# Performance work log

Hardware: AMD Instinct MI355X
Metric: run time of the kernel (lower is better)

## Reference

```python
import jax, jax.numpy as jnp
import numpy as np
from jax import lax

B = 16           # graphs per batch
N_PER = 4096     # points per graph (equal-sized graphs)
C_IN = 32        # in_channels
RATIO = 0.25
MAX_NBR = 32     # max_num_neighbors in radius()


def _xavier(key, fan_in, fan_out):
    lim = np.sqrt(6.0 / (fan_in + fan_out)).astype(np.float32)
    return jax.random.uniform(key, (fan_in, fan_out), jnp.float32, -lim, lim)


def setup_inputs() -> dict:
    key = jax.random.key(0)
    ks = jax.random.split(key, 16)
    x = jax.random.normal(ks[0], (B * N_PER, C_IN), jnp.float32)
    pos = jax.random.uniform(ks[1], (B * N_PER, 3), jnp.float32) * 20.0
    batch = jnp.repeat(jnp.arange(B, dtype=jnp.int64), N_PER)
    p = {
        'x': x, 'pos': pos, 'batch': batch,
        'scaler_mean': jnp.zeros((1, C_IN), jnp.float32),
        'scaler_std': jnp.ones((1, C_IN), jnp.float32),
        # SA1: Linear(32+3,64) -> Sigmoid -> Linear(64,128)
        'sa1_w1': _xavier(ks[2], C_IN + 3, 64), 'sa1_b1': jnp.zeros((64,), jnp.float32),
        'sa1_w2': _xavier(ks[3], 64, 128),      'sa1_b2': jnp.zeros((128,), jnp.float32),
        # SA2: Linear(128+3,128) -> Sigmoid -> Linear(128,256)
        'sa2_w1': _xavier(ks[4], 128 + 3, 128), 'sa2_b1': jnp.zeros((128,), jnp.float32),
        'sa2_w2': _xavier(ks[5], 128, 256),     'sa2_b2': jnp.zeros((256,), jnp.float32),
        # Global SA: Linear(256+3,256) -> Sigmoid -> Linear(256,512)
        'g_w1': _xavier(ks[6], 256 + 3, 256),   'g_b1': jnp.zeros((256,), jnp.float32),
        'g_w2': _xavier(ks[7], 256, 512),       'g_b2': jnp.zeros((512,), jnp.float32),
        # fc: Linear(512,256) -> Sigmoid -> Linear(256,128)
        'fc_w1': _xavier(ks[8], 512, 256),      'fc_b1': jnp.zeros((256,), jnp.float32),
        'fc_w2': _xavier(ks[9], 256, 128),      'fc_b2': jnp.zeros((128,), jnp.float32),
    }
    return p


def _fps(pos, k):
    # Farthest point sampling, deterministic start at index 0. pos: [B, n, 3] -> idx [B, k]
    pos = lax.stop_gradient(pos)
    d0 = jnp.sum((pos - pos[:, :1, :]) ** 2, -1)  # [B, n] dist^2 to start point

    def step(mind, _):
        nxt = jnp.argmax(mind, axis=1)                                  # [B]
        p = jnp.take_along_axis(pos, nxt[:, None, None], axis=1)        # [B,1,3]
        mind = jnp.minimum(mind, jnp.sum((pos - p) ** 2, -1))
        return mind, nxt

    _, rest = lax.scan(step, d0, None, length=k - 1)                    # [k-1, B]
    start = jnp.zeros((1, pos.shape[0]), rest.dtype)
    return jnp.concatenate([start, rest], 0).T                          # [B, k]


def _gather_nbr(v, nbr):
    # v: [B, n, C], nbr: [B, k, MAX_NBR] -> [B, k, MAX_NBR, C]
    return jax.vmap(lambda vb, nb: vb[nb])(v, nbr)


def _sa_module(x, pos, w1, b1, w2, b2, ratio, r):
    # PointNetConv (max aggregation) over a radius graph from FPS centers.
    Bb, n, _ = x.shape
    k = int(n * ratio)
    idx = _fps(pos, k)                                                  # [B, k]
    pos_dst = jnp.take_along_axis(pos, idx[:, :, None], axis=1)         # [B, k, 3]
    d2 = jnp.sum((pos_dst[:, :, None, :] - pos[:, None, :, :]) ** 2, -1)  # [B,k,n]
    masked = jnp.where(d2 <= r * r, d2, jnp.inf)
    negv, nbr = lax.top_k(-masked, MAX_NBR)                             # nearest <=32 within radius
    valid = jnp.isfinite(negv)                                          # [B,k,32]
    x_j = _gather_nbr(x, nbr)                                           # [B,k,32,C]
    rel = _gather_nbr(pos, nbr) - pos_dst[:, :, None, :]                # pos_j - pos_i
    feat = jnp.concatenate([x_j, rel], axis=-1)
    msg = jax.nn.sigmoid(feat @ w1 + b1) @ w2 + b2                      # [B,k,32,2h]
    msg = jnp.where(valid[..., None], msg, -jnp.inf)
    agg = jnp.max(msg, axis=2)                                          # max aggregation
    agg = jnp.where(jnp.isfinite(agg), agg, 0.0)  # (self is always a neighbor, defensive)
    return jax.nn.relu(agg), pos_dst


def reference(x, pos, batch, scaler_mean, scaler_std,
              sa1_w1, sa1_b1, sa1_w2, sa1_b2,
              sa2_w1, sa2_b1, sa2_w2, sa2_b2,
              g_w1, g_b1, g_w2, g_b2,
              fc_w1, fc_b1, fc_w2, fc_b2):
    x = (x - scaler_mean) / scaler_std
    xb = x.reshape(B, N_PER, -1)      # batch is sorted with N_PER points per graph
    pb = pos.reshape(B, N_PER, 3)
    xb, pb = _sa_module(xb, pb, sa1_w1, sa1_b1, sa1_w2, sa1_b2, RATIO, 2.0)
    xb, pb = _sa_module(xb, pb, sa2_w1, sa2_b1, sa2_w2, sa2_b2, RATIO, 4.0)
    # GlobalSAModule: relu(nn(cat[x, pos])) then global max pool
    h = jnp.concatenate([xb, pb], axis=-1)
    h = jax.nn.relu(jax.nn.sigmoid(h @ g_w1 + g_b1) @ g_w2 + g_b2)      # [B, 256, 512]
    g = jnp.max(h, axis=1)                                              # [B, 512]
    out = jax.nn.sigmoid(g @ fc_w1 + fc_b1) @ fc_w2 + fc_b2
    return jax.nn.relu(out)                                             # last_act='relu'
```

## Files before the change

kernel.cpp:

```cpp
#include <hip/hip_runtime.h>
#include <hip/hip_bf16.h>
#include <math.h>

namespace {

constexpr int NB   = 16;
constexpr int N1   = 4096;
constexpr int K1   = 1024;
constexpr int K2   = 256;
constexpr int MAXN = 32;
constexpr int RCAP = 448;

__device__ __forceinline__ float sigmoidf_(float x) {
  return 1.0f / (1.0f + __expf(-x));
}

__device__ __forceinline__ float readlane_f(float v, int l) {
  return __int_as_float(__builtin_amdgcn_readlane(__float_as_int(v), l));
}


#define FPS_DPP_STEP(CTRL)                                                     \
  {                                                                            \
    const unsigned olo =                                                       \
        (unsigned)__builtin_amdgcn_update_dpp(0, (int)lo, (CTRL), 0xF, 0xF, true); \
    const unsigned ohi =                                                       \
        (unsigned)__builtin_amdgcn_update_dpp(0, (int)hi, (CTRL), 0xF, 0xF, true); \
    const unsigned long long o = ((unsigned long long)ohi << 32) | olo;        \
    const unsigned long long cur = ((unsigned long long)hi << 32) | lo;        \
    if (o > cur) { lo = olo; hi = ohi; }                                       \
  }

template<int NPT>
__device__ __forceinline__ void fps_level(
    const float* __restrict__ sx, const float* __restrict__ sy,
    const float* __restrict__ sz, int k,
    float* __restrict__ selx, float* __restrict__ sely,
    float* __restrict__ selz,
    unsigned long long (*red)[4]) {
  const int t = threadIdx.x;
  const int lane = t & 63, wave = t >> 6;
  float px[NPT], py[NPT], pz[NPT], mind[NPT];
  unsigned niv[NPT];
  const float c0x = sx[0], c0y = sy[0], c0z = sz[0];
  unsigned long long best = 0;
#pragma unroll
  for (int i = 0; i < NPT; i++) {
    const int p = i * 256 + t;
    niv[i] = ~(unsigned)p;
    px[i] = sx[p]; py[i] = sy[p]; pz[i] = sz[p];
    const float dx = px[i] - c0x, dy = py[i] - c0y, dz = pz[i] - c0z;
    const float d2 = dx * dx + dy * dy + dz * dz;
    mind[i] = d2;
    const unsigned long long cand =
        ((unsigned long long)__float_as_uint(d2) << 32) | niv[i];
    if (cand > best) best = cand;
  }
  if (t == 0) { selx[0] = c0x; sely[0] = c0y; selz[0] = c0z; }
  for (int it = 1; it < k; it++) {
    unsigned lo = (unsigned)best, hi = (unsigned)(best >> 32);
    FPS_DPP_STEP(0x111)
    FPS_DPP_STEP(0x112)
    FPS_DPP_STEP(0x114)
    FPS_DPP_STEP(0x118)
    FPS_DPP_STEP(0x142)
    FPS_DPP_STEP(0x143)
    const int par = it & 1;
    if (lane == 63) red[par][wave] = ((unsigned long long)hi << 32) | lo;
    __syncthreads();
    const unsigned long long w0 = red[par][0], w1 = red[par][1];
    const unsigned long long w2 = red[par][2], w3 = red[par][3];
    const unsigned long long m01 = w0 > w1 ? w0 : w1;
    const unsigned long long m23 = w2 > w3 ? w2 : w3;
    const unsigned long long win = m01 > m23 ? m01 : m23;
    const int p = (int)(~(unsigned)win);
    const float nx = sx[p], ny = sy[p], nz = sz[p];
    if (t == 0) { selx[it] = nx; sely[it] = ny; selz[it] = nz; }
    best = 0;
#pragma unroll
    for (int i = 0; i < NPT; i++) {
      const float dx = px[i] - nx, dy = py[i] - ny, dz = pz[i] - nz;
      const float d2 = dx * dx + dy * dy + dz * dz;
      const float m = fminf(mind[i], d2);
      mind[i] = m;
      const unsigned long long cand =
          ((unsigned long long)__float_as_uint(m) << 32) | niv[i];
      if (cand > best) best = cand;
    }
  }
}

#undef FPS_DPP_STEP

__global__ __launch_bounds__(256) void fps_l1_kernel(
    const float* __restrict__ pos, float* __restrict__ posd1,
    unsigned int* __restrict__ gout) {
  __shared__ float sx[N1], sy[N1], sz[N1];
  __shared__ float s2x[K1], s2y[K1], s2z[K1];
  __shared__ __align__(16) unsigned long long red[2][4];
  const int b = blockIdx.x;
  const int t = threadIdx.x;
  gout[b * 512 + t] = 0u;
  gout[b * 512 + t + 256] = 0u;
  const float* pb = pos + (size_t)b * N1 * 3;
  for (int p = t; p < N1; p += 256) {
    sx[p] = pb[p * 3 + 0]; sy[p] = pb[p * 3 + 1]; sz[p] = pb[p * 3 + 2];
  }
  __syncthreads();
  fps_level<N1 / 256>(sx, sy, sz, K1, s2x, s2y, s2z, red);
  __syncthreads();
  float* o1 = posd1 + (size_t)b * K1 * 3;
  for (int i = t; i < K1; i += 256) {
    o1[i * 3 + 0] = s2x[i]; o1[i * 3 + 1] = s2y[i]; o1[i * 3 + 2] = s2z[i];
  }
}

struct RadSmem {
  float candd[4][RCAP];
  int   candi[4][RCAP];
};

template<int N>
__device__ __forceinline__ void radius_body(
    const float* __restrict__ pts, const float* __restrict__ ctr,
    int K, int CSTR, float r2, int* __restrict__ nbr,
    int* __restrict__ cnt_out, RadSmem& sm, int rb) {
  const int t = threadIdx.x;
  const int lane = t & 63, wave = t >> 6;
  const int bpg = K / 4;
  const int b = rb / bpg;
  const int ci = (rb % bpg) * 4 + wave;
  const float* pb = pts + (size_t)b * N * 3;
  const size_t cbase = ((size_t)b * CSTR + ci) * 3;
  const float cx = ctr[cbase + 0], cy = ctr[cbase + 1], cz = ctr[cbase + 2];
  int total = 0;
  for (int base = 0; base < N; base += 64) {
    const int p = base + lane;
    const float dx = pb[p * 3 + 0] - cx;
    const float dy = pb[p * 3 + 1] - cy;
    const float dz = pb[p * 3 + 2] - cz;
    const float d2 = dx * dx + dy * dy + dz * dz;
    const bool pred = d2 <= r2;
    const unsigned long long m = __ballot(pred);
    if (pred) {
      const int slot = total + __popcll(m & ((1ull << lane) - 1ull));
      if (slot < RCAP) { sm.candd[wave][slot] = d2; sm.candi[wave][slot] = p; }
    }
    total += __popcll(m);
  }
  if (total > RCAP) total = RCAP;
  int* nbp = nbr + ((size_t)b * K + ci) * MAXN;
  if (total <= MAXN) {
    if (lane < total) nbp[lane] = sm.candi[wave][lane];
  } else {
    for (int jj = 0; jj < MAXN; jj++) {
      float bvd = INFINITY; int bvi = 0x7fffffff; int bslot = 0;
      for (int s = lane; s < total; s += 64) {
        const float d = sm.candd[wave][s];
        const int i = sm.candi[wave][s];
        if (d < bvd || (d == bvd && i < bvi)) { bvd = d; bvi = i; bslot = s; }
      }
#pragma unroll
      for (int off = 32; off; off >>= 1) {
        const float od = __shfl_xor(bvd, off);
        const int   oi = __shfl_xor(bvi, off);
        const int   os = __shfl_xor(bslot, off);
        if (od < bvd || (od == bvd && oi < bvi)) { bvd = od; bvi = oi; bslot = os; }
      }
      if (lane == 0) { nbp[jj] = bvi; sm.candd[wave][bslot] = INFINITY; }
    }
  }
  if (lane == 0) cnt_out[(size_t)b * K + ci] = (total < MAXN) ? total : MAXN;
}

__global__ __launch_bounds__(256) void rad12_kernel(
    const float* __restrict__ pos, const float* __restrict__ posd1,
    int* __restrict__ nbr1, int* __restrict__ cnt1,
    int* __restrict__ nbr2, int* __restrict__ cnt2) {
  constexpr int NR1 = NB * K1 / 4;
  __shared__ __align__(16) RadSmem r;
  if (blockIdx.x < (unsigned)NR1) {
    radius_body<N1>(pos, posd1, K1, K1, 4.0f, nbr1, cnt1, r, blockIdx.x);
  } else {
    radius_body<K1>(posd1, posd1, K2, K1, 16.0f, nbr2, cnt2, r,
                    blockIdx.x - NR1);
  }
}

template<int CIN_T, int H, int COUT, bool SCALE>
__device__ __forceinline__ void sa_conv_body(
    const float* __restrict__ xin, const float* __restrict__ pts,
    const float* __restrict__ ctr, const int* __restrict__ nbr,
    const int* __restrict__ cnt,
    const float* __restrict__ w1, const float* __restrict__ b1,
    const float* __restrict__ w2, const float* __restrict__ b2,
    const float* __restrict__ smean, const float* __restrict__ sstd,
    int N, int K, int CSTR, float* __restrict__ xout,
    float* part , int bk) {
  constexpr int FIN  = CIN_T + 3;
  constexpr int KREG = (FIN + 63) / 64;
  constexpr int HREG = H / 64;
  constexpr int CREG = COUT / 64;
  constexpr int RPW  = MAXN / 4;
  const int t = threadIdx.x, lane = t & 63, wave = t >> 6;
  const int b = bk / K;
  const int V = cnt[bk];
  float m[CREG];
#pragma unroll
  for (int ck = 0; ck < CREG; ck++) m[ck] = -INFINITY;
  if (V > wave * RPW) {
    const int* nb = nbr + (size_t)bk * MAXN;
    const size_t crow = (size_t)b * CSTR + (bk - b * K);
    const float ctrx = ctr[crow * 3 + 0];
    const float ctry = ctr[crow * 3 + 1];
    const float ctrz = ctr[crow * 3 + 2];
    float sm = 0.0f, sd = 1.0f;
    if (SCALE && lane < CIN_T) { sm = smean[lane]; sd = sstd[lane]; }
    float fr[RPW][KREG];
#pragma unroll
    for (int r = 0; r < RPW; r++) {
      const int j = wave * RPW + r;
      const int p = (j < V) ? nb[j] : nb[0];
#pragma unroll
      for (int k2 = 0; k2 < KREG; k2++) {
        const int f = k2 * 64 + lane;
        float v = 0.0f;
        if (f < CIN_T) {
          v = xin[((size_t)b * N + p) * CIN_T + f];
          if constexpr (SCALE) v = (v - sm) / sd;
        } else if (f < FIN) {
          const int d = f - CIN_T;
          const float pv = pts[((size_t)b * N + p) * 3 + d];
          v = pv - (d == 0 ? ctrx : (d == 1 ? ctry : ctrz));
        }
        fr[r][k2] = v;
      }
    }
    float hh[RPW][HREG];
    {
      float acc[RPW][HREG];
#pragma unroll
      for (int r = 0; r < RPW; r++)
#pragma unroll
        for (int q = 0; q < HREG; q++) acc[r][q] = 0.0f;
#pragma unroll
      for (int k2 = 0; k2 < KREG; k2++) {
        const int lim = (FIN - k2 * 64) < 64 ? (FIN - k2 * 64) : 64;
        for (int fl = 0; fl < lim; fl++) {
          const int f = k2 * 64 + fl;
          float wv[HREG];
          if constexpr (HREG == 1) {
            wv[0] = w1[(size_t)f * H + lane];
          } else {
            const float2 w = *reinterpret_cast<const float2*>(
                &w1[(size_t)f * H + lane * 2]);
            wv[0] = w.x; wv[1] = w.y;
          }
#pragma unroll
          for (int r = 0; r < RPW; r++) {
            const float s = readlane_f(fr[r][k2], fl);
#pragma unroll
            for (int q = 0; q < HREG; q++) acc[r][q] = fmaf(s, wv[q], acc[r][q]);
          }
        }
      }
#pragma unroll
      for (int q = 0; q < HREG; q++) {
        const float bb = b1[lane * HREG + q];
#pragma unroll
        for (int r = 0; r < RPW; r++) hh[r][q] = sigmoidf_(acc[r][q] + bb);
      }
    }
    float acc2[RPW][CREG];
#pragma unroll
    for (int r = 0; r < RPW; r++)
#pragma unroll
      for (int q = 0; q < CREG; q++) acc2[r][q] = 0.0f;
    for (int hl = 0; hl < 64; hl++) {
#pragma unroll
      for (int q1 = 0; q1 < HREG; q1++) {
        const int h = hl * HREG + q1;
        float wv[CREG];
        if constexpr (CREG == 2) {
          const float2 w = *reinterpret_cast<const float2*>(
              &w2[(size_t)h * COUT + lane * 2]);
          wv[0] = w.x; wv[1] = w.y;
        } else {
          const float4 w = *reinterpret_cast<const float4*>(
              &w2[(size_t)h * COUT + lane * 4]);
          wv[0] = w.x; wv[1] = w.y; wv[2] = w.z; wv[3] = w.w;
        }
#pragma unroll
        for (int r = 0; r < RPW; r++) {
          const float s = readlane_f(hh[r][q1], hl);
#pragma unroll
          for (int q = 0; q < CREG; q++) acc2[r][q] = fmaf(s, wv[q], acc2[r][q]);
        }
      }
    }
#pragma unroll
    for (int r = 0; r < RPW; r++) {
      if (wave * RPW + r < V) {
#pragma unroll
        for (int q = 0; q < CREG; q++) m[q] = fmaxf(m[q], acc2[r][q]);
      }
    }
  }
#pragma unroll
  for (int q = 0; q < CREG; q++) part[wave * COUT + lane * CREG + q] = m[q];
  __syncthreads();
  if (t < COUT) {
    const float mm = fmaxf(fmaxf(part[0 * COUT + t], part[1 * COUT + t]),
                           fmaxf(part[2 * COUT + t], part[3 * COUT + t]));
    const float o = mm + b2[t];
    xout[(size_t)bk * COUT + t] = o > 0.0f ? o : 0.0f;
  }
}

__global__ __launch_bounds__(256) void conv1_kernel(
    const float* __restrict__ x, const float* __restrict__ pos,
    const float* __restrict__ posd1, const int* __restrict__ nbr1,
    const int* __restrict__ cnt1,
    const float* __restrict__ s1w1, const float* __restrict__ s1b1,
    const float* __restrict__ s1w2, const float* __restrict__ s1b2,
    const float* __restrict__ smean, const float* __restrict__ sstd,
    float* __restrict__ x1) {
  __shared__ __align__(16) float part[4 * 128];
  sa_conv_body<32, 64, 128, true>(x, pos, posd1, nbr1, cnt1,
                                  s1w1, s1b1, s1w2, s1b2, smean, sstd,
                                  N1, K1, K1, x1, part, blockIdx.x);
}

__global__ __launch_bounds__(256) void conv2_kernel(
    const float* __restrict__ x1, const float* __restrict__ posd1,
    const int* __restrict__ nbr2, const int* __restrict__ cnt2,
    const float* __restrict__ s2w1, const float* __restrict__ s2b1,
    const float* __restrict__ s2w2, const float* __restrict__ s2b2,
    float* __restrict__ x2) {
  __shared__ __align__(16) float part[4 * 256];
  sa_conv_body<128, 128, 256, false>(x1, posd1, posd1, nbr2, cnt2,
                                     s2w1, s2b1, s2w2, s2b2, nullptr, nullptr,
                                     K1, K2, K1, x2, part, blockIdx.x);
}

__global__ __launch_bounds__(256) void global_sa_kernel(
    const float* __restrict__ x2, const float* __restrict__ posd1,
    const float* __restrict__ gw1, const float* __restrict__ gb1,
    const float* __restrict__ gw2, const float* __restrict__ gb2,
    unsigned int* __restrict__ gout) {
  __shared__ float fin[4][259];
  __shared__ float s[4][256];
  const int t = threadIdx.x;
  const int blk = blockIdx.x;
  const int b = blk / 64;
  const int p0 = (blk % 64) * 4;
  for (int item = t; item < 4 * 259; item += 256) {
    const int p = item / 259, f = item - p * 259;
    const float v = (f < 256)
        ? x2[((size_t)b * 256 + p0 + p) * 256 + f]
        : posd1[((size_t)b * K1 + p0 + p) * 3 + (f - 256)];
    fin[p][f] = v;
  }
  __syncthreads();
  float acc[4] = {0.f, 0.f, 0.f, 0.f};
  for (int f = 0; f < 259; f++) {
    const float w = gw1[f * 256 + t];
#pragma unroll
    for (int p = 0; p < 4; p++) acc[p] = fmaf(fin[p][f], w, acc[p]);
  }
  const float bb = gb1[t];
#pragma unroll
  for (int p = 0; p < 4; p++) s[p][t] = sigmoidf_(acc[p] + bb);
  __syncthreads();
  float a0[4] = {0.f, 0.f, 0.f, 0.f}, a1[4] = {0.f, 0.f, 0.f, 0.f};
  for (int h = 0; h < 256; h++) {
    const float w0 = gw2[h * 512 + t];
    const float w1v = gw2[h * 512 + t + 256];
#pragma unroll
    for (int p = 0; p < 4; p++) {
      a0[p] = fmaf(s[p][h], w0, a0[p]);
      a1[p] = fmaf(s[p][h], w1v, a1[p]);
    }
  }
  const float b0 = gb2[t], b1v = gb2[t + 256];
  float m0 = 0.0f, m1 = 0.0f;
#pragma unroll
  for (int p = 0; p < 4; p++) {
    m0 = fmaxf(m0, fmaxf(a0[p] + b0, 0.0f));
    m1 = fmaxf(m1, fmaxf(a1[p] + b1v, 0.0f));
  }
  atomicMax(&gout[b * 512 + t], __float_as_uint(m0));
  atomicMax(&gout[b * 512 + t + 256], __float_as_uint(m1));
}

__global__ __launch_bounds__(256) void fc_kernel(
    const unsigned int* __restrict__ g,
    const float* __restrict__ fw1, const float* __restrict__ fb1,
    const float* __restrict__ fw2, const float* __restrict__ fb2,
    float* __restrict__ out) {
  __shared__ float gv[512];
  __shared__ float s[256];
  const int b = blockIdx.x, t = threadIdx.x;
  gv[t] = __uint_as_float(g[b * 512 + t]);
  gv[t + 256] = __uint_as_float(g[b * 512 + t + 256]);
  __syncthreads();
  float acc = 0.0f;
  for (int h = 0; h < 512; h++) acc = fmaf(gv[h], fw1[h * 256 + t], acc);
  s[t] = sigmoidf_(acc + fb1[t]);
  __syncthreads();
  if (t < 128) {
    float a2 = 0.0f;
    for (int h = 0; h < 256; h++) a2 = fmaf(s[h], fw2[h * 128 + t], a2);
    const float o = a2 + fb2[t];
    out[b * 128 + t] = o > 0.0f ? o : 0.0f;
  }
}

}

extern "C" void kernel_launch(void* const* d_in, const int* in_sizes, int n_in,
                              void* d_out, int out_size, void* d_ws, size_t ws_size,
                              hipStream_t stream) {
  (void)in_sizes; (void)n_in; (void)out_size; (void)ws_size;
  const float* x     = (const float*)d_in[0];
  const float* pos   = (const float*)d_in[1];
  const float* smean = (const float*)d_in[3];
  const float* sstd  = (const float*)d_in[4];
  const float* s1w1  = (const float*)d_in[5];
  const float* s1b1  = (const float*)d_in[6];
  const float* s1w2  = (const float*)d_in[7];
  const float* s1b2  = (const float*)d_in[8];
  const float* s2w1  = (const float*)d_in[9];
  const float* s2b1  = (const float*)d_in[10];
  const float* s2w2  = (const float*)d_in[11];
  const float* s2b2  = (const float*)d_in[12];
  const float* gw1   = (const float*)d_in[13];
  const float* gb1   = (const float*)d_in[14];
  const float* gw2   = (const float*)d_in[15];
  const float* gb2   = (const float*)d_in[16];
  const float* fw1   = (const float*)d_in[17];
  const float* fb1   = (const float*)d_in[18];
  const float* fw2   = (const float*)d_in[19];
  const float* fb2   = (const float*)d_in[20];

  char* ws = (char*)d_ws;
  size_t off = 0;
  auto take = [&](size_t bytes) -> char* {
    char* p = ws + off;
    off = (off + bytes + 255) & ~(size_t)255;
    return p;
  };
  float* posd1       = (float*)take((size_t)NB * K1 * 3 * 4);
  int*   nbr1        = (int*)take((size_t)NB * K1 * MAXN * 4);
  int*   cnt1        = (int*)take((size_t)NB * K1 * 4);
  float* x1          = (float*)take((size_t)NB * K1 * 128 * 4);
  int*   nbr2        = (int*)take((size_t)NB * K2 * MAXN * 4);
  int*   cnt2        = (int*)take((size_t)NB * K2 * 4);
  float* x2          = (float*)take((size_t)NB * K2 * 256 * 4);
  unsigned int* gbuf = (unsigned int*)take((size_t)NB * 512 * 4);

  hipLaunchKernelGGL(fps_l1_kernel, dim3(NB), dim3(256), 0, stream,
                     pos, posd1, gbuf);
  hipLaunchKernelGGL(rad12_kernel, dim3(NB * K1 / 4 + NB * K2 / 4), dim3(256), 0, stream,
                     pos, posd1, nbr1, cnt1, nbr2, cnt2);
  hipLaunchKernelGGL(conv1_kernel, dim3(NB * K1), dim3(256), 0, stream,
                     x, pos, posd1, nbr1, cnt1,
                     s1w1, s1b1, s1w2, s1b2, smean, sstd, x1);
  hipLaunchKernelGGL(conv2_kernel, dim3(NB * K2), dim3(256), 0, stream,
                     x1, posd1, nbr2, cnt2, s2w1, s2b1, s2w2, s2b2, x2);
  hipLaunchKernelGGL(global_sa_kernel, dim3(NB * 64), dim3(256), 0, stream,
                     x2, posd1, gw1, gb1, gw2, gb2, gbuf);
  hipLaunchKernelGGL(fc_kernel, dim3(NB), dim3(256), 0, stream,
                     gbuf, fw1, fb1, fw2, fb2, (float*)d_out);
}
```

Before: 1.160 ms.

## Store point and sampled-center coordinates as SoA arrays across all stages

The FPS kernel now writes the input positions and the sampled centers as separate x/y/z arrays instead of interleaved xyz. The radius search, both conv kernels and the global SA kernel read these structure-of-arrays buffers, so per-lane coordinate loads in the radius scan become unit-stride coalesced. The cost is an extra global write of all positions in the single-block-per-graph FPS kernel, plus the radius template on N becoming a runtime argument.

```diff
diff --git a/kernel.cpp b/kernel.cpp
--- a/kernel.cpp
+++ b/kernel.cpp
@@ -93,7 +93,9 @@
 #undef FPS_DPP_STEP
 
 __global__ __launch_bounds__(256) void fps_l1_kernel(
-    const float* __restrict__ pos, float* __restrict__ posd1,
+    const float* __restrict__ pos,
+    float* __restrict__ pxg, float* __restrict__ pyg, float* __restrict__ pzg,
+    float* __restrict__ d1x, float* __restrict__ d1y, float* __restrict__ d1z,
     unsigned int* __restrict__ gout) {
   __shared__ float sx[N1], sy[N1], sz[N1];
   __shared__ float s2x[K1], s2y[K1], s2z[K1];
@@ -109,9 +111,15 @@
   __syncthreads();
   fps_level<N1 / 256>(sx, sy, sz, K1, s2x, s2y, s2z, red);
   __syncthreads();
-  float* o1 = posd1 + (size_t)b * K1 * 3;
+  for (int p = t; p < N1; p += 256) {
+    pxg[(size_t)b * N1 + p] = sx[p];
+    pyg[(size_t)b * N1 + p] = sy[p];
+    pzg[(size_t)b * N1 + p] = sz[p];
+  }
   for (int i = t; i < K1; i += 256) {
-    o1[i * 3 + 0] = s2x[i]; o1[i * 3 + 1] = s2y[i]; o1[i * 3 + 2] = s2z[i];
+    d1x[(size_t)b * K1 + i] = s2x[i];
+    d1y[(size_t)b * K1 + i] = s2y[i];
+    d1z[(size_t)b * K1 + i] = s2z[i];
   }
 }
 
@@ -120,25 +128,26 @@
   int   candi[4][RCAP];
 };
 
-template<int N>
 __device__ __forceinline__ void radius_body(
-    const float* __restrict__ pts, const float* __restrict__ ctr,
-    int K, int CSTR, float r2, int* __restrict__ nbr,
-    int* __restrict__ cnt_out, RadSmem& sm, int rb) {
+    const float* __restrict__ ptsx, const float* __restrict__ ptsy,
+    const float* __restrict__ ptsz, int N,
+    const float* __restrict__ cxs, const float* __restrict__ cys,
+    const float* __restrict__ czs, int K, int CSTR, float r2,
+    int* __restrict__ nbr, int* __restrict__ cnt_out, RadSmem& sm, int rb) {
   const int t = threadIdx.x;
   const int lane = t & 63, wave = t >> 6;
   const int bpg = K / 4;
   const int b = rb / bpg;
   const int ci = (rb % bpg) * 4 + wave;
-  const float* pb = pts + (size_t)b * N * 3;
-  const size_t cbase = ((size_t)b * CSTR + ci) * 3;
-  const float cx = ctr[cbase + 0], cy = ctr[cbase + 1], cz = ctr[cbase + 2];
+  const size_t pbase = (size_t)b * N;
+  const size_t cbase = (size_t)b * CSTR + ci;
+  const float cx = cxs[cbase], cy = cys[cbase], cz = czs[cbase];
   int total = 0;
   for (int base = 0; base < N; base += 64) {
     const int p = base + lane;
-    const float dx = pb[p * 3 + 0] - cx;
-    const float dy = pb[p * 3 + 1] - cy;
-    const float dz = pb[p * 3 + 2] - cz;
+    const float dx = ptsx[pbase + p] - cx;
+    const float dy = ptsy[pbase + p] - cy;
+    const float dz = ptsz[pbase + p] - cz;
     const float d2 = dx * dx + dy * dy + dz * dz;
     const bool pred = d2 <= r2;
     const unsigned long long m = __ballot(pred);
@@ -174,24 +183,31 @@
 }
 
 __global__ __launch_bounds__(256) void rad12_kernel(
-    const float* __restrict__ pos, const float* __restrict__ posd1,
+    const float* __restrict__ pxg, const float* __restrict__ pyg,
+    const float* __restrict__ pzg,
+    const float* __restrict__ d1x, const float* __restrict__ d1y,
+    const float* __restrict__ d1z,
     int* __restrict__ nbr1, int* __restrict__ cnt1,
     int* __restrict__ nbr2, int* __restrict__ cnt2) {
   constexpr int NR1 = NB * K1 / 4;
   __shared__ __align__(16) RadSmem r;
   if (blockIdx.x < (unsigned)NR1) {
-    radius_body<N1>(pos, posd1, K1, K1, 4.0f, nbr1, cnt1, r, blockIdx.x);
+    radius_body(pxg, pyg, pzg, N1, d1x, d1y, d1z, K1, K1, 4.0f,
+                nbr1, cnt1, r, blockIdx.x);
   } else {
-    radius_body<K1>(posd1, posd1, K2, K1, 16.0f, nbr2, cnt2, r,
-                    blockIdx.x - NR1);
+    radius_body(d1x, d1y, d1z, K1, d1x, d1y, d1z, K2, K1, 16.0f,
+                nbr2, cnt2, r, blockIdx.x - NR1);
   }
 }
 
 template<int CIN_T, int H, int COUT, bool SCALE>
 __device__ __forceinline__ void sa_conv_body(
-    const float* __restrict__ xin, const float* __restrict__ pts,
-    const float* __restrict__ ctr, const int* __restrict__ nbr,
-    const int* __restrict__ cnt,
+    const float* __restrict__ xin,
+    const float* __restrict__ ptsx, const float* __restrict__ ptsy,
+    const float* __restrict__ ptsz,
+    const float* __restrict__ cxs, const float* __restrict__ cys,
+    const float* __restrict__ czs,
+    const int* __restrict__ nbr, const int* __restrict__ cnt,
     const float* __restrict__ w1, const float* __restrict__ b1,
     const float* __restrict__ w2, const float* __restrict__ b2,
     const float* __restrict__ smean, const float* __restrict__ sstd,
@@ -211,9 +227,9 @@
   if (V > wave * RPW) {
     const int* nb = nbr + (size_t)bk * MAXN;
     const size_t crow = (size_t)b * CSTR + (bk - b * K);
-    const float ctrx = ctr[crow * 3 + 0];
-    const float ctry = ctr[crow * 3 + 1];
-    const float ctrz = ctr[crow * 3 + 2];
+    const float ctrx = cxs[crow];
+    const float ctry = cys[crow];
+    const float ctrz = czs[crow];
     float sm = 0.0f, sd = 1.0f;
     if (SCALE && lane < CIN_T) { sm = smean[lane]; sd = sstd[lane]; }
     float fr[RPW][KREG];
@@ -230,7 +246,7 @@
           if constexpr (SCALE) v = (v - sm) / sd;
         } else if (f < FIN) {
           const int d = f - CIN_T;
-          const float pv = pts[((size_t)b * N + p) * 3 + d];
+          const float pv = (d == 0 ? ptsx : (d == 1 ? ptsy : ptsz))[(size_t)b * N + p];
           v = pv - (d == 0 ? ctrx : (d == 1 ? ctry : ctrz));
         }
         fr[r][k2] = v;
@@ -318,33 +334,42 @@
 }
 
 __global__ __launch_bounds__(256) void conv1_kernel(
-    const float* __restrict__ x, const float* __restrict__ pos,
-    const float* __restrict__ posd1, const int* __restrict__ nbr1,
-    const int* __restrict__ cnt1,
+    const float* __restrict__ x,
+    const float* __restrict__ pxg, const float* __restrict__ pyg,
+    const float* __restrict__ pzg,
+    const float* __restrict__ d1x, const float* __restrict__ d1y,
+    const float* __restrict__ d1z,
+    const int* __restrict__ nbr1, const int* __restrict__ cnt1,
     const float* __restrict__ s1w1, const float* __restrict__ s1b1,
     const float* __restrict__ s1w2, const float* __restrict__ s1b2,
     const float* __restrict__ smean, const float* __restrict__ sstd,
     float* __restrict__ x1) {
   __shared__ __align__(16) float part[4 * 128];
-  sa_conv_body<32, 64, 128, true>(x, pos, posd1, nbr1, cnt1,
-                                  s1w1, s1b1, s1w2, s1b2, smean, sstd,
-                                  N1, K1, K1, x1, part, blockIdx.x);
+  sa_conv_body<32, 64, 128, true>(x, pxg, pyg, pzg, d1x, d1y, d1z,
+                                  nbr1, cnt1, s1w1, s1b1, s1w2, s1b2,
+                                  smean, sstd, N1, K1, K1, x1, part,
+                                  blockIdx.x);
 }
 
 __global__ __launch_bounds__(256) void conv2_kernel(
-    const float* __restrict__ x1, const float* __restrict__ posd1,
+    const float* __restrict__ x1,
+    const float* __restrict__ d1x, const float* __restrict__ d1y,
+    const float* __restrict__ d1z,
     const int* __restrict__ nbr2, const int* __restrict__ cnt2,
     const float* __restrict__ s2w1, const float* __restrict__ s2b1,
     const float* __restrict__ s2w2, const float* __restrict__ s2b2,
     float* __restrict__ x2) {
   __shared__ __align__(16) float part[4 * 256];
-  sa_conv_body<128, 128, 256, false>(x1, posd1, posd1, nbr2, cnt2,
-                                     s2w1, s2b1, s2w2, s2b2, nullptr, nullptr,
-                                     K1, K2, K1, x2, part, blockIdx.x);
+  sa_conv_body<128, 128, 256, false>(x1, d1x, d1y, d1z, d1x, d1y, d1z,
+                                     nbr2, cnt2, s2w1, s2b1, s2w2, s2b2,
+                                     nullptr, nullptr, K1, K2, K1, x2, part,
+                                     blockIdx.x);
 }
 
 __global__ __launch_bounds__(256) void global_sa_kernel(
-    const float* __restrict__ x2, const float* __restrict__ posd1,
+    const float* __restrict__ x2,
+    const float* __restrict__ d1x, const float* __restrict__ d1y,
+    const float* __restrict__ d1z,
     const float* __restrict__ gw1, const float* __restrict__ gb1,
     const float* __restrict__ gw2, const float* __restrict__ gb2,
     unsigned int* __restrict__ gout) {
@@ -356,9 +381,13 @@
   const int p0 = (blk % 64) * 4;
   for (int item = t; item < 4 * 259; item += 256) {
     const int p = item / 259, f = item - p * 259;
-    const float v = (f < 256)
-        ? x2[((size_t)b * 256 + p0 + p) * 256 + f]
-        : posd1[((size_t)b * K1 + p0 + p) * 3 + (f - 256)];
+    float v;
+    if (f < 256) {
+      v = x2[((size_t)b * 256 + p0 + p) * 256 + f];
+    } else {
+      const int d = f - 256;
+      v = (d == 0 ? d1x : (d == 1 ? d1y : d1z))[(size_t)b * K1 + p0 + p];
+    }
     fin[p][f] = v;
   }
   __syncthreads();
@@ -450,7 +479,12 @@
     off = (off + bytes + 255) & ~(size_t)255;
     return p;
   };
-  float* posd1       = (float*)take((size_t)NB * K1 * 3 * 4);
+  float* pxg         = (float*)take((size_t)NB * N1 * 4);
+  float* pyg         = (float*)take((size_t)NB * N1 * 4);
+  float* pzg         = (float*)take((size_t)NB * N1 * 4);
+  float* d1x         = (float*)take((size_t)NB * K1 * 4);
+  float* d1y         = (float*)take((size_t)NB * K1 * 4);
+  float* d1z         = (float*)take((size_t)NB * K1 * 4);
   int*   nbr1        = (int*)take((size_t)NB * K1 * MAXN * 4);
   int*   cnt1        = (int*)take((size_t)NB * K1 * 4);
   float* x1          = (float*)take((size_t)NB * K1 * 128 * 4);
@@ -460,16 +494,17 @@
   unsigned int* gbuf = (unsigned int*)take((size_t)NB * 512 * 4);
 
   hipLaunchKernelGGL(fps_l1_kernel, dim3(NB), dim3(256), 0, stream,
-                     pos, posd1, gbuf);
+                     pos, pxg, pyg, pzg, d1x, d1y, d1z, gbuf);
   hipLaunchKernelGGL(rad12_kernel, dim3(NB * K1 / 4 + NB * K2 / 4), dim3(256), 0, stream,
-                     pos, posd1, nbr1, cnt1, nbr2, cnt2);
+                     pxg, pyg, pzg, d1x, d1y, d1z, nbr1, cnt1, nbr2, cnt2);
   hipLaunchKernelGGL(conv1_kernel, dim3(NB * K1), dim3(256), 0, stream,
-                     x, pos, posd1, nbr1, cnt1,
+                     x, pxg, pyg, pzg, d1x, d1y, d1z, nbr1, cnt1,
                      s1w1, s1b1, s1w2, s1b2, smean, sstd, x1);
   hipLaunchKernelGGL(conv2_kernel, dim3(NB * K2), dim3(256), 0, stream,
-                     x1, posd1, nbr2, cnt2, s2w1, s2b1, s2w2, s2b2, x2);
+                     x1, d1x, d1y, d1z, nbr2, cnt2,
+                     s2w1, s2b1, s2w2, s2b2, x2);
   hipLaunchKernelGGL(global_sa_kernel, dim3(NB * 64), dim3(256), 0, stream,
-                     x2, posd1, gw1, gb1, gw2, gb2, gbuf);
+                     x2, d1x, d1y, d1z, gw1, gb1, gw2, gb2, gbuf);
   hipLaunchKernelGGL(fc_kernel, dim3(NB), dim3(256), 0, stream,
                      gbuf, fw1, fb1, fw2, fb2, (float*)d_out);
 }
```

Measured after the change: 1.150 ms, median of 3. No clear change (-0.9%).
